# Kernel tuning notes

Hardware: AMD Instinct MI355X
Metric: run time of the kernel (lower is better)

The kernel has to match this reference:

```python
import jax, jax.numpy as jnp
from jax import lax
import numpy as np

H = 64
IN = 7
EPS = 1e-5


def _lstm_layer(x_seq, Wih, Whh, bih, bhh):
    # x_seq: [B, T, D] -> returns [B, T, H]; PyTorch gate order i,f,g,o
    B = x_seq.shape[0]
    b = bih + bhh
    x_tbd = jnp.swapaxes(x_seq, 0, 1)  # [T, B, D]
    # precompute input projections for all timesteps (one big GEMM)
    xproj = jnp.einsum('tbd,gd->tbg', x_tbd, Wih) + b  # [T, B, 4H]

    def step(carry, xp_t):
        h, c = carry
        gates = xp_t + h @ Whh.T  # [B, 4H]
        i, f, g, o = jnp.split(gates, 4, axis=-1)
        i = jax.nn.sigmoid(i)
        f = jax.nn.sigmoid(f)
        g = jnp.tanh(g)
        o = jax.nn.sigmoid(o)
        c = f * c + i * g
        h = o * jnp.tanh(c)
        return (h, c), h

    init = (jnp.zeros((B, H), x_seq.dtype), jnp.zeros((B, H), x_seq.dtype))
    _, hs = lax.scan(step, init, xproj)  # hs: [T, B, H]
    return jnp.swapaxes(hs, 0, 1)


def setup_inputs() -> dict:
    key = jax.random.key(0)
    ks = jax.random.split(key, 16)
    s = 1.0 / np.sqrt(H)
    u = lambda k, shape: jax.random.uniform(k, shape, jnp.float32, -s, s)
    inp = {
        'x': jax.random.normal(ks[0], (256, IN, 2048), jnp.float32),
        'Wih0': u(ks[1], (4 * H, IN)),
        'Whh0': u(ks[2], (4 * H, H)),
        'bih0': u(ks[3], (4 * H,)),
        'bhh0': u(ks[4], (4 * H,)),
        'Wih1': u(ks[5], (4 * H, H)),
        'Whh1': u(ks[6], (4 * H, H)),
        'bih1': u(ks[7], (4 * H,)),
        'bhh1': u(ks[8], (4 * H,)),
        'W1': u(ks[9], (10, H)),
        'b1': u(ks[10], (10,)),
        'gamma': jnp.ones((10,), jnp.float32),
        'beta': jnp.zeros((10,), jnp.float32),
        'rm': jax.random.normal(ks[11], (10,), jnp.float32) * 0.1,
        'rv': jax.random.uniform(ks[12], (10,), jnp.float32, 0.5, 1.5),
        'W2': u(ks[13], (1, 10)),
        'b2': u(ks[14], (1,)),
    }
    return inp


def reference(x, Wih0, Whh0, bih0, bhh0, Wih1, Whh1, bih1, bhh1,
              W1, b1, gamma, beta, rm, rv, W2, b2):
    # x: [B, 7, T] -> permute to [B, T, 7] (batch_first LSTM input)
    xs = jnp.transpose(x, (0, 2, 1))
    h0 = _lstm_layer(xs, Wih0, Whh0, bih0, bhh0)   # [B, T, H]
    h1 = _lstm_layer(h0, Wih1, Whh1, bih1, bhh1)   # [B, T, H] (dropout=0.05 inactive in eval)
    last = h1[:, -1, :]                            # [B, H]
    y = last @ W1.T + b1                           # [B, 10]
    y = (y - rm) * lax.rsqrt(rv + EPS) * gamma + beta  # BN1d eval mode
    y = jax.nn.relu(y)
    return y @ W2.T + b2                           # [B, 1]
```

## Files before the change

kernel.cpp:

```cpp
#include <hip/hip_runtime.h>
#include <math.h>

#define HH  64
#define TT  2048
#define IND 7
#define NT  256

typedef _Float16 half_t;
typedef _Float16 h2v __attribute__((ext_vector_type(2)));
typedef _Float16 h8v __attribute__((ext_vector_type(8)));
typedef unsigned int u2v __attribute__((ext_vector_type(2)));

#define LOG2E 1.44269504088896f

#define S2C(V, I) __builtin_shufflevector(V, V, 2*(I), 2*(I)+1)

__device__ __forceinline__ float fdot2(h2v a, h2v b, float c) {
#if __has_builtin(__builtin_amdgcn_fdot2)
    return __builtin_amdgcn_fdot2(a, b, c, false);
#else
    return fmaf((float)a.x, (float)b.x, fmaf((float)a.y, (float)b.y, c));
#endif
}

__device__ __forceinline__ float exp2_fast(float x) {
#if __has_builtin(__builtin_amdgcn_exp2f)
    return __builtin_amdgcn_exp2f(x);
#else
    return exp2f(x);
#endif
}
__device__ __forceinline__ float rcp_fast(float x) {
#if __has_builtin(__builtin_amdgcn_rcpf)
    return __builtin_amdgcn_rcpf(x);
#else
    return __fdividef(1.0f, x);
#endif
}

__device__ __forceinline__ float partner32(float x, int hi) {
#if __has_builtin(__builtin_amdgcn_permlane32_swap)
    u2v r = __builtin_amdgcn_permlane32_swap(__float_as_uint(x), __float_as_uint(x), false, false);
    return hi ? __uint_as_float(r.x) : __uint_as_float(r.y);
#else
    return __shfl_xor(x, 32);
#endif
}

__device__ __forceinline__ float sig2(float ahat) {
    return rcp_fast(1.0f + exp2_fast(-ahat));
}
__device__ __forceinline__ float tanh2(float c) {
    float e = exp2_fast(c * (-2.0f * LOG2E));
    return fmaf(2.0f, rcp_fast(1.0f + e), -1.0f);
}

#define DOT4(ACC, W, H) \
    ACC = fdot2((W)[0], S2C(H, 0), ACC); \
    ACC = fdot2((W)[1], S2C(H, 1), ACC); \
    ACC = fdot2((W)[2], S2C(H, 2), ACC); \
    ACC = fdot2((W)[3], S2C(H, 3), ACC);

__global__ __launch_bounds__(NT) __attribute__((amdgpu_waves_per_eu(1, 1)))
void lstm2_fused(
    const float* __restrict__ x,
    const float* __restrict__ Wih0,
    const float* __restrict__ Whh0,
    const float* __restrict__ bih0, const float* __restrict__ bhh0,
    const float* __restrict__ Wih1,
    const float* __restrict__ Whh1,
    const float* __restrict__ bih1, const float* __restrict__ bhh1,
    const float* __restrict__ W1,
    const float* __restrict__ b1v,
    const float* __restrict__ gmma, const float* __restrict__ beta,
    const float* __restrict__ rm,   const float* __restrict__ rv,
    const float* __restrict__ W2,
    const float* __restrict__ b2,
    float* __restrict__ out)
{
    const int b    = blockIdx.x;
    const int tid  = threadIdx.x;
    const int wave = tid >> 6;
    const int lane = tid & 63;

    __shared__ __align__(16) half_t xTh[TT][8];
    __shared__ __align__(16) half_t h0s[2][HH];
    __shared__ __align__(16) half_t h1s[2][HH];
    __shared__ float yv[10];

    {
        const float* xg = x + (size_t)b * (IND * TT);
        for (int i = tid; i < IND * TT; i += NT) {
            int d = i >> 11;
            int t = i & (TT - 1);
            xTh[t][d] = (half_t)xg[i];
        }
        for (int t = tid; t < TT; t += NT) xTh[t][7] = (half_t)0.0f;
        if (tid < HH) {
            h0s[1][tid] = (half_t)0.0f;
            h1s[0][tid] = (half_t)0.0f;
            h1s[1][tid] = (half_t)0.0f;
        }
    }

    __syncthreads();

    if (wave < 2) {
        const int j  = ((wave & 1) << 5) | (lane & 31);
        const int kh = lane >> 5;

        h2v wh[4][16];
        h2v xw[4][4];
        float bg[4];
        #pragma unroll
        for (int s = 0; s < 4; ++s) {
            const int g = (s << 6) | j;
            const float sc = (s == 2) ? 2.0f * LOG2E : LOG2E;
            const float* pw = Whh0 + g * HH + 32 * kh;
            #pragma unroll
            for (int r = 0; r < 16; ++r)
                wh[s][r] = h2v{(half_t)(pw[2*r] * sc), (half_t)(pw[2*r+1] * sc)};
            float t8[8];
            #pragma unroll
            for (int d = 0; d < 8; ++d)
                t8[d] = (d < IND && kh) ? Wih0[g * IND + d] * sc : 0.0f;
            #pragma unroll
            for (int r = 0; r < 4; ++r)
                xw[s][r] = h2v{(half_t)t8[2*r], (half_t)t8[2*r+1]};
            bg[s] = (kh == 0) ? (bih0[g] + bhh0[g]) * sc : 0.0f;
        }

        float c0 = 0.0f;

        for (int tick = 0; tick <= TT; ++tick) {
            const int p = tick & 1;
            if (tick < TT) {
                const h8v* hp = (const h8v*)&h0s[p ^ 1][32 * kh];
                h8v H0 = hp[0], H1 = hp[1], H2 = hp[2], H3 = hp[3];
                h8v XV = *((const h8v*)&xTh[tick][0]);
                float fa[4], fb[4];
                #pragma unroll
                for (int s = 0; s < 4; ++s) {
                    float a = bg[s], bb = 0.0f;
                    DOT4(a,  &wh[s][0],  H0)
                    DOT4(a,  &wh[s][4],  H1)
                    DOT4(bb, &wh[s][8],  H2)
                    DOT4(bb, &wh[s][12], H3)
                    DOT4(a,  &xw[s][0],  XV)
                    fa[s] = a; fb[s] = bb;
                }
                float fi, ff, fg, fo;
                { float pr = fa[0] + fb[0]; fi = pr + partner32(pr, kh); }
                { float pr = fa[1] + fb[1]; ff = pr + partner32(pr, kh); }
                { float pr = fa[2] + fb[2]; fg = pr + partner32(pr, kh); }
                { float pr = fa[3] + fb[3]; fo = pr + partner32(pr, kh); }
                float iv = sig2(fi);
                float fv = sig2(ff);
                float gv = fmaf(2.0f, sig2(fg), -1.0f);
                float ov = sig2(fo);
                c0 = fmaf(fv, c0, iv * gv);
                float hn = ov * tanh2(c0);
                if (kh == 0) h0s[p][j] = (half_t)hn;
            }
            __syncthreads();
        }
    } else {
        const int j  = ((wave & 1) << 5) | (lane & 31);
        const int mh = lane >> 5;

        h2v wt[4][32];
        float bg[4];
        const float* WB = mh ? Whh1 : Wih1;
        #pragma unroll
        for (int s = 0; s < 4; ++s) {
            const int g = (s << 6) | j;
            const float sc = (s == 2) ? 2.0f * LOG2E : LOG2E;
            const float* pw = WB + g * HH;
            #pragma unroll
            for (int r = 0; r < 32; ++r)
                wt[s][r] = h2v{(half_t)(pw[2*r] * sc), (half_t)(pw[2*r+1] * sc)};
            bg[s] = (mh == 0) ? (bih1[g] + bhh1[g]) * sc : 0.0f;
        }

        float c1 = 0.0f;

        for (int tick = 0; tick <= TT; ++tick) {
            const int p = tick & 1;
            if (tick > 0) {
                const h8v* hp = mh ? (const h8v*)&h1s[p ^ 1][0]
                                   : (const h8v*)&h0s[p ^ 1][0];
                h8v H0 = hp[0], H1 = hp[1], H2 = hp[2], H3 = hp[3];
                h8v H4 = hp[4], H5 = hp[5], H6 = hp[6], H7 = hp[7];
                float fa[4], fb[4];
                #pragma unroll
                for (int s = 0; s < 4; ++s) {
                    float a = bg[s], bb = 0.0f;
                    DOT4(a,  &wt[s][0],  H0)
                    DOT4(a,  &wt[s][4],  H1)
                    DOT4(a,  &wt[s][8],  H2)
                    DOT4(a,  &wt[s][12], H3)
                    DOT4(bb, &wt[s][16], H4)
                    DOT4(bb, &wt[s][20], H5)
                    DOT4(bb, &wt[s][24], H6)
                    DOT4(bb, &wt[s][28], H7)
                    fa[s] = a; fb[s] = bb;
                }
                float fi, ff, fg, fo;
                { float pr = fa[0] + fb[0]; fi = pr + partner32(pr, mh); }
                { float pr = fa[1] + fb[1]; ff = pr + partner32(pr, mh); }
                { float pr = fa[2] + fb[2]; fg = pr + partner32(pr, mh); }
                { float pr = fa[3] + fb[3]; fo = pr + partner32(pr, mh); }
                float iv = sig2(fi);
                float fv = sig2(ff);
                float gv = fmaf(2.0f, sig2(fg), -1.0f);
                float ov = sig2(fo);
                c1 = fmaf(fv, c1, iv * gv);
                float hn = ov * tanh2(c1);
                if (mh == 0) h1s[p][j] = (half_t)hn;
            }
            __syncthreads();
        }
    }

    if (tid < 10) {
        float y = b1v[tid];
        #pragma unroll
        for (int k = 0; k < HH; ++k) y += W1[tid * HH + k] * (float)h1s[0][k];
        y = (y - rm[tid]) * rsqrtf(rv[tid] + 1e-5f) * gmma[tid] + beta[tid];
        y = fmaxf(y, 0.0f);
        yv[tid] = y * W2[tid];
    }
    __syncthreads();
    if (tid == 0) {
        float sacc = b2[0];
        #pragma unroll
        for (int k = 0; k < 10; ++k) sacc += yv[k];
        out[b] = sacc;
    }
}

extern "C" void kernel_launch(void* const* d_in, const int* in_sizes, int n_in,
                              void* d_out, int out_size, void* d_ws, size_t ws_size,
                              hipStream_t stream) {
    const float* x    = (const float*)d_in[0];
    const float* Wih0 = (const float*)d_in[1];
    const float* Whh0 = (const float*)d_in[2];
    const float* bih0 = (const float*)d_in[3];
    const float* bhh0 = (const float*)d_in[4];
    const float* Wih1 = (const float*)d_in[5];
    const float* Whh1 = (const float*)d_in[6];
    const float* bih1 = (const float*)d_in[7];
    const float* bhh1 = (const float*)d_in[8];
    const float* W1   = (const float*)d_in[9];
    const float* b1   = (const float*)d_in[10];
    const float* gmma = (const float*)d_in[11];
    const float* beta = (const float*)d_in[12];
    const float* rm   = (const float*)d_in[13];
    const float* rv   = (const float*)d_in[14];
    const float* W2   = (const float*)d_in[15];
    const float* b2   = (const float*)d_in[16];

    const int B = in_sizes[0] / (IND * TT);

    lstm2_fused<<<dim3(B), dim3(NT), 0, stream>>>(
        x, Wih0, Whh0, bih0, bhh0, Wih1, Whh1, bih1, bhh1,
        W1, b1, gmma, beta, rm, rv, W2, b2, (float*)d_out);
}
```

Measured before the change: 955.9 us.

## Split each hidden unit's gate dot products across four lanes with DPP reduction

Doubles the block to 512 threads so each layer uses four waves, and splits each hidden unit's dot product four ways instead of two. A DPP quad-permute plus the 32-lane swap combines the partial sums. This halves per-lane FMA chains and weight registers on the serial per-timestep critical path. The cost is an extra cross-lane reduction step per gate, more waves joining each barrier, and a waves_per_eu hint change that lowers the register budget.

```diff
diff --git a/kernel.cpp b/kernel.cpp
--- a/kernel.cpp
+++ b/kernel.cpp
@@ -4,7 +4,7 @@
 #define HH  64
 #define TT  2048
 #define IND 7
-#define NT  256
+#define NT  512
 
 typedef _Float16 half_t;
 typedef _Float16 h2v __attribute__((ext_vector_type(2)));
@@ -45,6 +45,17 @@
 #else
     return __shfl_xor(x, 32);
 #endif
+}
+
+template <int CTRL>
+__device__ __forceinline__ float qperm(float x) {
+    return __int_as_float(__builtin_amdgcn_update_dpp(0, __float_as_int(x), CTRL, 0xf, 0xf, true));
+}
+#define QP_X1 0xB1
+
+__device__ __forceinline__ float qreduce(float pr, int qb1) {
+    float s1 = pr + qperm<QP_X1>(pr);
+    return s1 + partner32(s1, qb1);
 }
 
 __device__ __forceinline__ float sig2(float ahat) {
@@ -61,7 +72,7 @@
     ACC = fdot2((W)[2], S2C(H, 2), ACC); \
     ACC = fdot2((W)[3], S2C(H, 3), ACC);
 
-__global__ __launch_bounds__(NT) __attribute__((amdgpu_waves_per_eu(1, 1)))
+__global__ __launch_bounds__(NT) __attribute__((amdgpu_waves_per_eu(2, 2)))
 void lstm2_fused(
     const float* __restrict__ x,
     const float* __restrict__ Wih0,
@@ -82,6 +93,12 @@
     const int tid  = threadIdx.x;
     const int wave = tid >> 6;
     const int lane = tid & 63;
+    const int ul   = (lane >> 1) & 15;
+    const int j    = ((wave & 3) << 4) | ul;
+    const int qb0  = lane & 1;
+    const int qb1  = lane >> 5;
+    const int qq   = (qb1 << 1) | qb0;
+    const bool pub = ((lane & 33) == 0);
 
     __shared__ __align__(16) half_t xTh[TT][8];
     __shared__ __align__(16) half_t h0s[2][HH];
@@ -105,29 +122,26 @@
 
     __syncthreads();
 
-    if (wave < 2) {
-        const int j  = ((wave & 1) << 5) | (lane & 31);
-        const int kh = lane >> 5;
-
-        h2v wh[4][16];
+    if (wave < 4) {
+        h2v wh[4][8];
         h2v xw[4][4];
         float bg[4];
         #pragma unroll
         for (int s = 0; s < 4; ++s) {
             const int g = (s << 6) | j;
             const float sc = (s == 2) ? 2.0f * LOG2E : LOG2E;
-            const float* pw = Whh0 + g * HH + 32 * kh;
-            #pragma unroll
-            for (int r = 0; r < 16; ++r)
+            const float* pw = Whh0 + g * HH + 16 * qq;
+            #pragma unroll
+            for (int r = 0; r < 8; ++r)
                 wh[s][r] = h2v{(half_t)(pw[2*r] * sc), (half_t)(pw[2*r+1] * sc)};
             float t8[8];
             #pragma unroll
             for (int d = 0; d < 8; ++d)
-                t8[d] = (d < IND && kh) ? Wih0[g * IND + d] * sc : 0.0f;
+                t8[d] = (d < IND && qq == 3) ? Wih0[g * IND + d] * sc : 0.0f;
             #pragma unroll
             for (int r = 0; r < 4; ++r)
                 xw[s][r] = h2v{(half_t)t8[2*r], (half_t)t8[2*r+1]};
-            bg[s] = (kh == 0) ? (bih0[g] + bhh0[g]) * sc : 0.0f;
+            bg[s] = (qq == 0) ? (bih0[g] + bhh0[g]) * sc : 0.0f;
         }
 
         float c0 = 0.0f;
@@ -135,51 +149,47 @@
         for (int tick = 0; tick <= TT; ++tick) {
             const int p = tick & 1;
             if (tick < TT) {
-                const h8v* hp = (const h8v*)&h0s[p ^ 1][32 * kh];
-                h8v H0 = hp[0], H1 = hp[1], H2 = hp[2], H3 = hp[3];
+                const h8v* hp = (const h8v*)&h0s[p ^ 1][16 * qq];
+                h8v H0 = hp[0], H1 = hp[1];
                 h8v XV = *((const h8v*)&xTh[tick][0]);
-                float fa[4], fb[4];
+                float fr[4];
                 #pragma unroll
                 for (int s = 0; s < 4; ++s) {
                     float a = bg[s], bb = 0.0f;
-                    DOT4(a,  &wh[s][0],  H0)
-                    DOT4(a,  &wh[s][4],  H1)
-                    DOT4(bb, &wh[s][8],  H2)
-                    DOT4(bb, &wh[s][12], H3)
-                    DOT4(a,  &xw[s][0],  XV)
-                    fa[s] = a; fb[s] = bb;
+                    DOT4(a,  &wh[s][0], H0)
+                    DOT4(bb, &wh[s][4], H1)
+                    DOT4(a,  &xw[s][0], XV)
+                    fr[s] = a + bb;
                 }
-                float fi, ff, fg, fo;
-                { float pr = fa[0] + fb[0]; fi = pr + partner32(pr, kh); }
-                { float pr = fa[1] + fb[1]; ff = pr + partner32(pr, kh); }
-                { float pr = fa[2] + fb[2]; fg = pr + partner32(pr, kh); }
-                { float pr = fa[3] + fb[3]; fo = pr + partner32(pr, kh); }
+                float fi = qreduce(fr[0], qb1);
+                float ff = qreduce(fr[1], qb1);
+                float fg = qreduce(fr[2], qb1);
+                float fo = qreduce(fr[3], qb1);
                 float iv = sig2(fi);
                 float fv = sig2(ff);
                 float gv = fmaf(2.0f, sig2(fg), -1.0f);
                 float ov = sig2(fo);
                 c0 = fmaf(fv, c0, iv * gv);
                 float hn = ov * tanh2(c0);
-                if (kh == 0) h0s[p][j] = (half_t)hn;
+                if (pub) h0s[p][j] = (half_t)hn;
             }
             __syncthreads();
         }
     } else {
-        const int j  = ((wave & 1) << 5) | (lane & 31);
-        const int mh = lane >> 5;
-
-        h2v wt[4][32];
+        const int mh = qb0;
+        const int kh = qb1;
+        h2v wt[4][16];
         float bg[4];
         const float* WB = mh ? Whh1 : Wih1;
         #pragma unroll
         for (int s = 0; s < 4; ++s) {
             const int g = (s << 6) | j;
             const float sc = (s == 2) ? 2.0f * LOG2E : LOG2E;
-            const float* pw = WB + g * HH;
-            #pragma unroll
-            for (int r = 0; r < 32; ++r)
+            const float* pw = WB + g * HH + 32 * kh;
+            #pragma unroll
+            for (int r = 0; r < 16; ++r)
                 wt[s][r] = h2v{(half_t)(pw[2*r] * sc), (half_t)(pw[2*r+1] * sc)};
-            bg[s] = (mh == 0) ? (bih1[g] + bhh1[g]) * sc : 0.0f;
+            bg[s] = (qq == 0) ? (bih1[g] + bhh1[g]) * sc : 0.0f;
         }
 
         float c1 = 0.0f;
@@ -187,36 +197,30 @@
         for (int tick = 0; tick <= TT; ++tick) {
             const int p = tick & 1;
             if (tick > 0) {
-                const h8v* hp = mh ? (const h8v*)&h1s[p ^ 1][0]
-                                   : (const h8v*)&h0s[p ^ 1][0];
+                const h8v* hp = mh ? (const h8v*)&h1s[p ^ 1][32 * kh]
+                                   : (const h8v*)&h0s[p ^ 1][32 * kh];
                 h8v H0 = hp[0], H1 = hp[1], H2 = hp[2], H3 = hp[3];
-                h8v H4 = hp[4], H5 = hp[5], H6 = hp[6], H7 = hp[7];
-                float fa[4], fb[4];
+                float fr[4];
                 #pragma unroll
                 for (int s = 0; s < 4; ++s) {
                     float a = bg[s], bb = 0.0f;
                     DOT4(a,  &wt[s][0],  H0)
-                    DOT4(a,  &wt[s][4],  H1)
+                    DOT4(bb, &wt[s][4],  H1)
                     DOT4(a,  &wt[s][8],  H2)
-                    DOT4(a,  &wt[s][12], H3)
-                    DOT4(bb, &wt[s][16], H4)
-                    DOT4(bb, &wt[s][20], H5)
-                    DOT4(bb, &wt[s][24], H6)
-                    DOT4(bb, &wt[s][28], H7)
-                    fa[s] = a; fb[s] = bb;
+                    DOT4(bb, &wt[s][12], H3)
+                    fr[s] = a + bb;
                 }
-                float fi, ff, fg, fo;
-                { float pr = fa[0] + fb[0]; fi = pr + partner32(pr, mh); }
-                { float pr = fa[1] + fb[1]; ff = pr + partner32(pr, mh); }
-                { float pr = fa[2] + fb[2]; fg = pr + partner32(pr, mh); }
-                { float pr = fa[3] + fb[3]; fo = pr + partner32(pr, mh); }
+                float fi = qreduce(fr[0], qb1);
+                float ff = qreduce(fr[1], qb1);
+                float fg = qreduce(fr[2], qb1);
+                float fo = qreduce(fr[3], qb1);
                 float iv = sig2(fi);
                 float fv = sig2(ff);
                 float gv = fmaf(2.0f, sig2(fg), -1.0f);
                 float ov = sig2(fo);
                 c1 = fmaf(fv, c1, iv * gv);
                 float hn = ov * tanh2(c1);
-                if (mh == 0) h1s[p][j] = (half_t)hn;
+                if (pub) h1s[p][j] = (half_t)hn;
             }
             __syncthreads();
         }
```

After: 1.186 ms. +24.0%, slower.

## Deepen layer pipeline with 4-slot h0 ring and prefetched operands

Applied to the files above, without the earlier changes.

Layer-1 waves now split the reduction over k halves for both input and recurrent weights, as layer 0 does, instead of splitting by matrix. Layer-0 output is kept in a 4-slot ring, so layer 1 can load h0 one tick ahead into registers before the barrier and run two ticks behind. The x input for the next step is prefetched. Dot products use four independent accumulators to shorten the dependency chains. The aim is to take LDS loads and long FMA chains off the per-step critical path between barriers, at the cost of one extra tick and more registers.

```diff
diff --git a/kernel.cpp b/kernel.cpp
--- a/kernel.cpp
+++ b/kernel.cpp
@@ -38,10 +38,10 @@
 #endif
 }
 
-__device__ __forceinline__ float partner32(float x, int hi) {
+__device__ __forceinline__ float partner32(float x, int kh) {
 #if __has_builtin(__builtin_amdgcn_permlane32_swap)
     u2v r = __builtin_amdgcn_permlane32_swap(__float_as_uint(x), __float_as_uint(x), false, false);
-    return hi ? __uint_as_float(r.x) : __uint_as_float(r.y);
+    return kh ? __uint_as_float(r.x) : __uint_as_float(r.y);
 #else
     return __shfl_xor(x, 32);
 #endif
@@ -82,10 +82,13 @@
     const int tid  = threadIdx.x;
     const int wave = tid >> 6;
     const int lane = tid & 63;
+    const int kh   = lane >> 5;
+    const int j    = ((wave & 1) << 5) | (lane & 31);
+    const bool pub = (kh == 0);
 
     __shared__ __align__(16) half_t xTh[TT][8];
-    __shared__ __align__(16) half_t h0s[2][HH];
-    __shared__ __align__(16) half_t h1s[2][HH];
+    __shared__ __align__(16) half_t h0r[4][HH];
+    __shared__ __align__(16) half_t h1r[2][HH];
     __shared__ float yv[10];
 
     {
@@ -97,18 +100,14 @@
         }
         for (int t = tid; t < TT; t += NT) xTh[t][7] = (half_t)0.0f;
         if (tid < HH) {
-            h0s[1][tid] = (half_t)0.0f;
-            h1s[0][tid] = (half_t)0.0f;
-            h1s[1][tid] = (half_t)0.0f;
+            h0r[3][tid] = (half_t)0.0f;
+            h1r[1][tid] = (half_t)0.0f;
         }
     }
 
     __syncthreads();
 
     if (wave < 2) {
-        const int j  = ((wave & 1) << 5) | (lane & 31);
-        const int kh = lane >> 5;
-
         h2v wh[4][16];
         h2v xw[4][4];
         float bg[4];
@@ -131,92 +130,91 @@
         }
 
         float c0 = 0.0f;
-
-        for (int tick = 0; tick <= TT; ++tick) {
-            const int p = tick & 1;
+        h8v XV = *((const h8v*)&xTh[0][0]);
+
+        for (int tick = 0; tick <= TT + 1; ++tick) {
             if (tick < TT) {
-                const h8v* hp = (const h8v*)&h0s[p ^ 1][32 * kh];
+                const h8v* hp = (const h8v*)&h0r[(tick - 1) & 3][32 * kh];
                 h8v H0 = hp[0], H1 = hp[1], H2 = hp[2], H3 = hp[3];
-                h8v XV = *((const h8v*)&xTh[tick][0]);
-                float fa[4], fb[4];
+                float fr[4];
                 #pragma unroll
                 for (int s = 0; s < 4; ++s) {
-                    float a = bg[s], bb = 0.0f;
-                    DOT4(a,  &wh[s][0],  H0)
-                    DOT4(a,  &wh[s][4],  H1)
-                    DOT4(bb, &wh[s][8],  H2)
-                    DOT4(bb, &wh[s][12], H3)
-                    DOT4(a,  &xw[s][0],  XV)
-                    fa[s] = a; fb[s] = bb;
+                    float a0 = bg[s], a1 = 0.f, a2 = 0.f, a3 = 0.f;
+                    DOT4(a0, &xw[s][0], XV)
+                    DOT4(a0, &wh[s][0],  H0)
+                    DOT4(a1, &wh[s][4],  H1)
+                    DOT4(a2, &wh[s][8],  H2)
+                    DOT4(a3, &wh[s][12], H3)
+                    fr[s] = (a0 + a1) + (a2 + a3);
                 }
-                float fi, ff, fg, fo;
-                { float pr = fa[0] + fb[0]; fi = pr + partner32(pr, kh); }
-                { float pr = fa[1] + fb[1]; ff = pr + partner32(pr, kh); }
-                { float pr = fa[2] + fb[2]; fg = pr + partner32(pr, kh); }
-                { float pr = fa[3] + fb[3]; fo = pr + partner32(pr, kh); }
+                float fi = fr[0] + partner32(fr[0], kh);
+                float ff = fr[1] + partner32(fr[1], kh);
+                float fg = fr[2] + partner32(fr[2], kh);
+                float fo = fr[3] + partner32(fr[3], kh);
                 float iv = sig2(fi);
                 float fv = sig2(ff);
                 float gv = fmaf(2.0f, sig2(fg), -1.0f);
                 float ov = sig2(fo);
                 c0 = fmaf(fv, c0, iv * gv);
                 float hn = ov * tanh2(c0);
-                if (kh == 0) h0s[p][j] = (half_t)hn;
+                if (pub) h0r[tick & 3][j] = (half_t)hn;
+                XV = *((const h8v*)&xTh[(tick + 1) & (TT - 1)][0]);
             }
             __syncthreads();
         }
     } else {
-        const int j  = ((wave & 1) << 5) | (lane & 31);
-        const int mh = lane >> 5;
-
-        h2v wt[4][32];
+        h2v wi[4][16], wh[4][16];
         float bg[4];
-        const float* WB = mh ? Whh1 : Wih1;
         #pragma unroll
         for (int s = 0; s < 4; ++s) {
             const int g = (s << 6) | j;
             const float sc = (s == 2) ? 2.0f * LOG2E : LOG2E;
-            const float* pw = WB + g * HH;
-            #pragma unroll
-            for (int r = 0; r < 32; ++r)
-                wt[s][r] = h2v{(half_t)(pw[2*r] * sc), (half_t)(pw[2*r+1] * sc)};
-            bg[s] = (mh == 0) ? (bih1[g] + bhh1[g]) * sc : 0.0f;
+            const float* p0 = Wih1 + g * HH + 32 * kh;
+            const float* p1 = Whh1 + g * HH + 32 * kh;
+            #pragma unroll
+            for (int r = 0; r < 16; ++r) {
+                wi[s][r] = h2v{(half_t)(p0[2*r] * sc), (half_t)(p0[2*r+1] * sc)};
+                wh[s][r] = h2v{(half_t)(p1[2*r] * sc), (half_t)(p1[2*r+1] * sc)};
+            }
+            bg[s] = (kh == 0) ? (bih1[g] + bhh1[g]) * sc : 0.0f;
         }
 
         float c1 = 0.0f;
-
-        for (int tick = 0; tick <= TT; ++tick) {
-            const int p = tick & 1;
-            if (tick > 0) {
-                const h8v* hp = mh ? (const h8v*)&h1s[p ^ 1][0]
-                                   : (const h8v*)&h0s[p ^ 1][0];
-                h8v H0 = hp[0], H1 = hp[1], H2 = hp[2], H3 = hp[3];
-                h8v H4 = hp[4], H5 = hp[5], H6 = hp[6], H7 = hp[7];
-                float fa[4], fb[4];
+        h8v P0 = {}, P1 = {}, P2 = {}, P3 = {};
+
+        for (int tick = 0; tick <= TT + 1; ++tick) {
+            if (tick >= 2) {
+                const h8v* q = (const h8v*)&h1r[(tick - 3) & 1][32 * kh];
+                h8v Q0 = q[0], Q1 = q[1], Q2 = q[2], Q3 = q[3];
+                float fr[4];
                 #pragma unroll
                 for (int s = 0; s < 4; ++s) {
-                    float a = bg[s], bb = 0.0f;
-                    DOT4(a,  &wt[s][0],  H0)
-                    DOT4(a,  &wt[s][4],  H1)
-                    DOT4(a,  &wt[s][8],  H2)
-                    DOT4(a,  &wt[s][12], H3)
-                    DOT4(bb, &wt[s][16], H4)
-                    DOT4(bb, &wt[s][20], H5)
-                    DOT4(bb, &wt[s][24], H6)
-                    DOT4(bb, &wt[s][28], H7)
-                    fa[s] = a; fb[s] = bb;
+                    float a0 = bg[s], a1 = 0.f, a2 = 0.f, a3 = 0.f;
+                    DOT4(a0, &wi[s][0],  P0)
+                    DOT4(a1, &wi[s][4],  P1)
+                    DOT4(a2, &wi[s][8],  P2)
+                    DOT4(a3, &wi[s][12], P3)
+                    DOT4(a0, &wh[s][0],  Q0)
+                    DOT4(a1, &wh[s][4],  Q1)
+                    DOT4(a2, &wh[s][8],  Q2)
+                    DOT4(a3, &wh[s][12], Q3)
+                    fr[s] = (a0 + a1) + (a2 + a3);
                 }
-                float fi, ff, fg, fo;
-                { float pr = fa[0] + fb[0]; fi = pr + partner32(pr, mh); }
-                { float pr = fa[1] + fb[1]; ff = pr + partner32(pr, mh); }
-                { float pr = fa[2] + fb[2]; fg = pr + partner32(pr, mh); }
-                { float pr = fa[3] + fb[3]; fo = pr + partner32(pr, mh); }
+                float fi = fr[0] + partner32(fr[0], kh);
+                float ff = fr[1] + partner32(fr[1], kh);
+                float fg = fr[2] + partner32(fr[2], kh);
+                float fo = fr[3] + partner32(fr[3], kh);
                 float iv = sig2(fi);
                 float fv = sig2(ff);
                 float gv = fmaf(2.0f, sig2(fg), -1.0f);
                 float ov = sig2(fo);
                 c1 = fmaf(fv, c1, iv * gv);
                 float hn = ov * tanh2(c1);
-                if (mh == 0) h1s[p][j] = (half_t)hn;
+                if (pub) h1r[tick & 1][j] = (half_t)hn;
+            }
+            if (tick >= 1) {
+                const h8v* pp = (const h8v*)&h0r[(tick - 1) & 3][32 * kh];
+                P0 = pp[0]; P1 = pp[1]; P2 = pp[2]; P3 = pp[3];
             }
             __syncthreads();
         }
@@ -225,7 +223,7 @@
     if (tid < 10) {
         float y = b1v[tid];
         #pragma unroll
-        for (int k = 0; k < HH; ++k) y += W1[tid * HH + k] * (float)h1s[0][k];
+        for (int k = 0; k < HH; ++k) y += W1[tid * HH + k] * (float)h1r[1][k];
         y = (y - rm[tid]) * rsqrtf(rv[tid] + 1e-5f) * gmma[tid] + beta[tid];
         y = fmaxf(y, 0.0f);
         yv[tid] = y * W2[tid];
```

Measured after the change: 1.040 ms. +8.8%, slower.
